# Kernel optimization log

Measured on AMD Instinct MI355X. Metric: run time of the kernel, lower is better.

## Reference

```python
import jax, jax.numpy as jnp
import numpy as np

B, L, D, H = 2, 2048, 1024, 16
DK = D // H
DFF = 4 * D
EPS = 1e-5  # torch LayerNorm default


def setup_inputs() -> dict:
    key = jax.random.key(0)
    ks = jax.random.split(key, 12)
    w = lambda k, shp: (jax.random.normal(k, shp, jnp.float32) * 0.02)
    return {
        "x": jax.random.normal(ks[0], (B, L, D), jnp.float32),
        "y": jax.random.normal(ks[1], (B, L, D), jnp.float32),
        "Wq": w(ks[2], (D, D)), "bq": jnp.zeros((D,), jnp.float32),
        "Wk": w(ks[3], (D, D)), "bk": jnp.zeros((D,), jnp.float32),
        "Wv": w(ks[4], (D, D)), "bv": jnp.zeros((D,), jnp.float32),
        "Wo": w(ks[5], (D, D)), "bo": jnp.zeros((D,), jnp.float32),
        "W1": w(ks[6], (D, DFF)), "b1": jnp.zeros((DFF,), jnp.float32),
        "W2": w(ks[7], (DFF, D)), "b2": jnp.zeros((D,), jnp.float32),
        "ln1_w": jnp.ones((L, D), jnp.float32), "ln1_b": jnp.zeros((L, D), jnp.float32),
        "ln2_w": jnp.ones((L, D), jnp.float32), "ln2_b": jnp.zeros((L, D), jnp.float32),
    }


def _layernorm2d(t, w, b):
    # nn.LayerNorm(normalized_shape=[L, D]): normalize jointly over last two dims
    mu = jnp.mean(t, axis=(-2, -1), keepdims=True)
    var = jnp.mean((t - mu) ** 2, axis=(-2, -1), keepdims=True)
    return (t - mu) * jax.lax.rsqrt(var + EPS) * w + b


def _attention(q_in, kv_in, Wq, bq, Wk, bk, Wv, bv, Wo, bo):
    split = lambda t: t.reshape(B, L, H, DK).transpose(0, 2, 1, 3)  # [B,H,L,DK]
    q = split(q_in @ Wq + bq)
    k = split(kv_in @ Wk + bk)
    v = split(kv_in @ Wv + bv)
    scores = jnp.einsum("bhqd,bhkd->bhqk", q, k) / (DK ** 0.5)
    # NOTE: original applies torch.tril to SCORES (zeroes upper triangle,
    # NOT -inf), so future positions still contribute exp(0)=1 in softmax.
    scores = jnp.tril(scores)
    p_attn = jax.nn.softmax(scores, axis=-1)
    out = jnp.einsum("bhqk,bhkd->bhqd", p_attn, v)
    out = out.transpose(0, 2, 1, 3).reshape(B, L, D)
    return out @ Wo + bo


def reference(x, y, Wq, bq, Wk, bk, Wv, bv, Wo, bo, W1, b1, W2, b2,
              ln1_w, ln1_b, ln2_w, ln2_b):
    # sublayer 0: pre-norm y, attention(query=x, key=value=norm(y)), residual
    y1 = y + _attention(x, _layernorm2d(y, ln1_w, ln1_b),
                        Wq, bq, Wk, bk, Wv, bv, Wo, bo)
    # sublayer 1: pre-norm, FFN (dropout inactive in eval), residual
    h = jax.nn.relu(_layernorm2d(y1, ln2_w, ln2_b) @ W1 + b1)
    return y1 + h @ W2 + b2
```

## Files before the change

### kernel.cpp

```cpp
#include <hip/hip_runtime.h>
#include <math.h>

#define B 2
#define L 2048
#define D 1024
#define H 16
#define DK 64
#define DFF 4096
#define EPS 1e-5f

typedef short short8 __attribute__((ext_vector_type(8)));
typedef short short4v __attribute__((ext_vector_type(4)));
typedef float float4v __attribute__((ext_vector_type(4)));
typedef unsigned int u32;

__device__ inline short f2bf(float f) {
    unsigned u = __builtin_bit_cast(unsigned, f);
    u += 0x7fffu + ((u >> 16) & 1u);
    return (short)(u >> 16);
}

__device__ inline float bf2f(short s) {
    unsigned u = ((unsigned)(unsigned short)s) << 16;
    return __builtin_bit_cast(float, u);
}

#define GLOAD_LDS16(gp, lp)                                                  \
    __builtin_amdgcn_global_load_lds(                                        \
        (const __attribute__((address_space(1))) u32*)(const void*)(gp),     \
        (__attribute__((address_space(3))) u32*)(void*)(lp), 16, 0, 0)

__device__ inline void xcd_remap(int& bx, int& by) {
    const int nbx = gridDim.x, nby = gridDim.y;
    const int orig = blockIdx.x + nbx * blockIdx.y;
    const int k = orig & 7, j = orig >> 3;
    const int nyc = nby >> 3;
    bx = j % nbx;
    by = k * nyc + j / nbx;
}


__global__ __launch_bounds__(256) void red_partial(const float* __restrict__ X,
                                                   float* __restrict__ part) {
    int b = blockIdx.y;
    const float4* p = (const float4*)(X + (size_t)b * L * D);
    float s = 0.f, ss = 0.f;
    for (int idx = blockIdx.x * 256 + threadIdx.x; idx < L * D / 4; idx += 256 * 256) {
        float4 v = p[idx];
        s += v.x + v.y + v.z + v.w;
        ss += v.x * v.x + v.y * v.y + v.z * v.z + v.w * v.w;
    }
    __shared__ float sh0[256], sh1[256];
    sh0[threadIdx.x] = s; sh1[threadIdx.x] = ss;
    __syncthreads();
    for (int o = 128; o; o >>= 1) {
        if (threadIdx.x < o) {
            sh0[threadIdx.x] += sh0[threadIdx.x + o];
            sh1[threadIdx.x] += sh1[threadIdx.x + o];
        }
        __syncthreads();
    }
    if (threadIdx.x == 0) {
        part[(b * 256 + blockIdx.x) * 2 + 0] = sh0[0];
        part[(b * 256 + blockIdx.x) * 2 + 1] = sh1[0];    }
}

__global__ __launch_bounds__(256) void red_final(const float* __restrict__ part,
                                                 float* __restrict__ stats) {
    int b = blockIdx.x;
    float s = part[(b * 256 + threadIdx.x) * 2 + 0];
    float ss = part[(b * 256 + threadIdx.x) * 2 + 1];
    __shared__ float sh0[256], sh1[256];
    sh0[threadIdx.x] = s; sh1[threadIdx.x] = ss;
    __syncthreads();
    for (int o = 128; o; o >>= 1) {
        if (threadIdx.x < o) {
            sh0[threadIdx.x] += sh0[threadIdx.x + o];
            sh1[threadIdx.x] += sh1[threadIdx.x + o];
        }
        __syncthreads();
    }
    if (threadIdx.x == 0) {
        const float invN = 1.f / (float)(L * D);
        float mu = sh0[0] * invN;
        float var = sh1[0] * invN - mu * mu;
        stats[b * 2 + 0] = mu;
        stats[b * 2 + 1] = rsqrtf(var + EPS);
    }
}

__global__ __launch_bounds__(256) void ln_apply_bf(const float* __restrict__ X,
                                                   const float* __restrict__ W,
                                                   const float* __restrict__ Bb,
                                                   const float* __restrict__ stats,
                                                   short* __restrict__ Yn) {
    int b = blockIdx.y;
    float mu = stats[b * 2 + 0];
    float rstd = stats[b * 2 + 1];
    size_t e = (size_t)(blockIdx.x * 256 + threadIdx.x) * 4;
    const float4 xv = *(const float4*)(X + (size_t)b * L * D + e);
    const float4 wv = *(const float4*)(W + e);
    const float4 bv = *(const float4*)(Bb + e);
    short4v o;
    o[0] = f2bf((xv.x - mu) * rstd * wv.x + bv.x);
    o[1] = f2bf((xv.y - mu) * rstd * wv.y + bv.y);
    o[2] = f2bf((xv.z - mu) * rstd * wv.z + bv.z);
    o[3] = f2bf((xv.w - mu) * rstd * wv.w + bv.w);
    *(short4v*)(Yn + (size_t)b * L * D + e) = o;
}

__global__ __launch_bounds__(256) void convert_bf(const float* __restrict__ X,
                                                  short* __restrict__ Y) {
    size_t e = (size_t)(blockIdx.x * 256 + threadIdx.x) * 4;
    const float4 v = *(const float4*)(X + e);
    short4v o = {f2bf(v.x), f2bf(v.y), f2bf(v.z), f2bf(v.w)};
    *(short4v*)(Y + e) = o;
}

__global__ __launch_bounds__(256) void wt_transpose(const float* __restrict__ W,
                                                    short* __restrict__ WT,
                                                    int K, int N) {
    __shared__ short tile[32][33];
    const int t = threadIdx.x;
    const int tx = t & 31, ty = t >> 5;
    const int k0 = blockIdx.y * 32, n0 = blockIdx.x * 32;
#pragma unroll
    for (int i = 0; i < 4; ++i) {
        const int k = ty + i * 8;
        tile[k][tx] = f2bf(W[(size_t)(k0 + k) * N + n0 + tx]);
    }
    __syncthreads();
#pragma unroll
    for (int i = 0; i < 4; ++i) {
        const int n = ty + i * 8;
        WT[(size_t)(n0 + n) * K + k0 + tx] = tile[tx][n];
    }
}


__global__ __launch_bounds__(256) void gemm_cv128(const short* __restrict__ A,
                                                  const short* __restrict__ BT,
                                                  const float* __restrict__ bias,
                                                  const float* __restrict__ Res,
                                                  void* __restrict__ Cout,
                                                  int M, int N, int K, int flags) {
    __shared__ short As[2][128 * 64];
    __shared__ short Bs[2][128 * 64];
    const int t = threadIdx.x;
    const int wave = t >> 6, lane = t & 63;
    const int m16 = lane & 15, q4 = lane >> 4;
    int bx, by;
    xcd_remap(bx, by);
    const int m0 = by * 128, n0 = bx * 128;
    const int wm = (wave >> 1) * 64, wn = (wave & 1) * 64;
    const int xorm = m16 & 7;

    float4v acc[4][4];
#pragma unroll
    for (int i = 0; i < 4; ++i)
#pragma unroll
        for (int j = 0; j < 4; ++j) acc[i][j] = (float4v){0.f, 0.f, 0.f, 0.f};

    auto stage = [&](int buf, int k0) {
#pragma unroll
        for (int p = 0; p < 4; ++p) {
            const int s = p * 256 + t;
            const int row = s >> 3;
            const int col = ((s & 7) ^ (row & 7)) * 8;
            short* lds = &As[buf][(p * 256 + wave * 64) * 8];
            GLOAD_LDS16(A + (size_t)(m0 + row) * K + k0 + col, lds);
        }
#pragma unroll
        for (int p = 0; p < 4; ++p) {
            const int s = p * 256 + t;
            const int row = s >> 3;
            const int col = ((s & 7) ^ (row & 7)) * 8;
            short* lds = &Bs[buf][(p * 256 + wave * 64) * 8];
            GLOAD_LDS16(BT + (size_t)(n0 + row) * K + k0 + col, lds);
        }
    };

    auto compute = [&](int buf) {
#pragma unroll
        for (int kk = 0; kk < 2; ++kk) {
            const int slot = ((kk * 4 + q4) ^ xorm) * 8;
            short8 af[4], bf[4];
#pragma unroll
            for (int mi = 0; mi < 4; ++mi)
                af[mi] = *(const short8*)&As[buf][(wm + mi * 16 + m16) * 64 + slot];
#pragma unroll
            for (int ni = 0; ni < 4; ++ni)
                bf[ni] = *(const short8*)&Bs[buf][(wn + ni * 16 + m16) * 64 + slot];
#pragma unroll
            for (int mi = 0; mi < 4; ++mi)
#pragma unroll
                for (int ni = 0; ni < 4; ++ni)
                    acc[mi][ni] = __builtin_amdgcn_mfma_f32_16x16x32_bf16(
                        af[mi], bf[ni], acc[mi][ni], 0, 0, 0);
        }
    };

    const int nt = K >> 6;
    stage(0, 0);
    for (int ti = 0; ti < nt; ++ti) {
        const int cur = ti & 1;
        if (ti + 1 < nt) {
            stage(cur ^ 1, (ti + 1) << 6);
            asm volatile("s_waitcnt vmcnt(8)" ::: "memory");
        } else {
            asm volatile("s_waitcnt vmcnt(0)" ::: "memory");
        }
        __builtin_amdgcn_s_barrier();
        __builtin_amdgcn_sched_barrier(0);
        compute(cur);
        __builtin_amdgcn_s_barrier();
    }

#pragma unroll
    for (int mi = 0; mi < 4; ++mi)
#pragma unroll
        for (int ni = 0; ni < 4; ++ni) {
            const int col = n0 + wn + ni * 16 + m16;
            const float bb = bias[col];
#pragma unroll
            for (int r = 0; r < 4; ++r) {
                const int row = m0 + wm + mi * 16 + q4 * 4 + r;
                float v = acc[mi][ni][r] + bb;
                if (Res) v += Res[(size_t)row * N + col];
                if (flags & 1) v = fmaxf(v, 0.f);
                if (flags & 2)
                    ((short*)Cout)[(size_t)row * N + col] = f2bf(v);
                else
                    ((float*)Cout)[(size_t)row * N + col] = v;
            }
        }
}

__global__ __launch_bounds__(512) void gemm_cv256(const short* __restrict__ A,
                                                  const short* __restrict__ BT,
                                                  const float* __restrict__ bias,
                                                  const float* __restrict__ Res,
                                                  void* __restrict__ Cout,
                                                  int M, int N, int K, int flags) {
    __shared__ short As[2][256 * 64];
    __shared__ short Bs[2][256 * 64];
    const int t = threadIdx.x;
    const int wave = t >> 6, lane = t & 63;
    const int m16 = lane & 15, q4 = lane >> 4;
    int bx, by;
    xcd_remap(bx, by);
    const int m0 = by * 256, n0 = bx * 256;
    const int wm = (wave >> 2) * 128, wn = (wave & 3) * 64;
    const int xorm = m16 & 7;

    float4v acc[8][4];
#pragma unroll
    for (int i = 0; i < 8; ++i)
#pragma unroll
        for (int j = 0; j < 4; ++j) acc[i][j] = (float4v){0.f, 0.f, 0.f, 0.f};

    auto stage = [&](int buf, int k0) {
#pragma unroll
        for (int p = 0; p < 4; ++p) {
            const int s = p * 512 + t;
            const int row = s >> 3;
            const int col = ((s & 7) ^ (row & 7)) * 8;
            short* lds = &As[buf][(p * 512 + wave * 64) * 8];
            GLOAD_LDS16(A + (size_t)(m0 + row) * K + k0 + col, lds);
        }
#pragma unroll
        for (int p = 0; p < 4; ++p) {
            const int s = p * 512 + t;
            const int row = s >> 3;
            const int col = ((s & 7) ^ (row & 7)) * 8;
            short* lds = &Bs[buf][(p * 512 + wave * 64) * 8];
            GLOAD_LDS16(BT + (size_t)(n0 + row) * K + k0 + col, lds);
        }
    };

    auto compute = [&](int buf) {
#pragma unroll
        for (int kk = 0; kk < 2; ++kk) {
            const int slot = ((kk * 4 + q4) ^ xorm) * 8;
            short8 af[8], bf[4];
#pragma unroll
            for (int mi = 0; mi < 8; ++mi)
                af[mi] = *(const short8*)&As[buf][(wm + mi * 16 + m16) * 64 + slot];
#pragma unroll
            for (int ni = 0; ni < 4; ++ni)
                bf[ni] = *(const short8*)&Bs[buf][(wn + ni * 16 + m16) * 64 + slot];
#pragma unroll
            for (int mi = 0; mi < 8; ++mi)
#pragma unroll
                for (int ni = 0; ni < 4; ++ni)
                    acc[mi][ni] = __builtin_amdgcn_mfma_f32_16x16x32_bf16(
                        af[mi], bf[ni], acc[mi][ni], 0, 0, 0);
        }
    };

    const int nt = K >> 6;
    stage(0, 0);
    for (int ti = 0; ti < nt; ++ti) {
        const int cur = ti & 1;
        if (ti + 1 < nt) {
            stage(cur ^ 1, (ti + 1) << 6);
            asm volatile("s_waitcnt vmcnt(8)" ::: "memory");
        } else {
            asm volatile("s_waitcnt vmcnt(0)" ::: "memory");
        }
        __builtin_amdgcn_s_barrier();
        __builtin_amdgcn_sched_barrier(0);
        compute(cur);
        __builtin_amdgcn_s_barrier();
    }

#pragma unroll
    for (int mi = 0; mi < 8; ++mi)
#pragma unroll
        for (int ni = 0; ni < 4; ++ni) {
            const int col = n0 + wn + ni * 16 + m16;
            const float bb = bias[col];
#pragma unroll
            for (int r = 0; r < 4; ++r) {
                const int row = m0 + wm + mi * 16 + q4 * 4 + r;
                float v = acc[mi][ni][r] + bb;
                if (Res) v += Res[(size_t)row * N + col];
                if (flags & 1) v = fmaxf(v, 0.f);
                if (flags & 2)
                    ((short*)Cout)[(size_t)row * N + col] = f2bf(v);
                else
                    ((float*)Cout)[(size_t)row * N + col] = v;
            }
        }
}


#define ASTR 72
#define SKV (2 * D)

__global__ __launch_bounds__(256) void v_tilesum(const short* __restrict__ KVg,
                                                 float* __restrict__ Vtile) {
    const int bh = blockIdx.x >> 5;
    const int kt = blockIdx.x & 31;
    const int b = bh >> 4, h = bh & (H - 1);
    const size_t baseV = (size_t)b * L * SKV + (size_t)h * DK + D;
    const int d = threadIdx.x & 63, g = threadIdx.x >> 6;
    float s = 0.f;
    for (int j = g * 16; j < g * 16 + 16; ++j)
        s += bf2f(KVg[baseV + (size_t)(kt * 64 + j) * SKV + d]);
    __shared__ float sh[4][64];
    sh[g][d] = s;
    __syncthreads();
    if (threadIdx.x < 64)
        Vtile[((size_t)bh * 32 + kt) * 64 + d] = sh[0][d] + sh[1][d] + sh[2][d] + sh[3][d];
}

__global__ __launch_bounds__(64) void v_suffix(const float* __restrict__ Vtile,
                                               float* __restrict__ Vsuf) {
    const int bh = blockIdx.x;
    const int d = threadIdx.x;
    float s = 0.f;
    Vsuf[((size_t)bh * 33 + 32) * 64 + d] = 0.f;
    for (int kt = 31; kt >= 0; --kt) {
        s += Vtile[((size_t)bh * 32 + kt) * 64 + d];
        Vsuf[((size_t)bh * 33 + kt) * 64 + d] = s;
    }
}


__device__ inline void attn_stage_load(const short* __restrict__ KVg,
                                       size_t baseK, int kt0, int sj, int sd8,
                                       short8* kr, short8* vr) {
#pragma unroll
    for (int rep = 0; rep < 2; ++rep) {
        const int j = rep * 32 + sj;
        const size_t g = baseK + (size_t)(kt0 + j) * SKV + sd8;
        kr[rep] = *(const short8*)(KVg + g);
        vr[rep] = *(const short8*)(KVg + g + D);
    }
}

__device__ inline void attn_stage_write(short* __restrict__ KbB,
                                        short* __restrict__ VtB,
                                        int sj, int sd8,
                                        const short8* kr, const short8* vr) {
    const int sm = sd8 >> 3;
#pragma unroll
    for (int rep = 0; rep < 2; ++rep) {
        const int j = rep * 32 + sj;
        *(short8*)&KbB[j * ASTR + sd8] = kr[rep];
        const int jsw = ((((j >> 3) ^ sm) << 3) | (j & 7));
#pragma unroll
        for (int i = 0; i < 8; ++i) VtB[(sd8 + i) * ASTR + jsw] = vr[rep][i];
    }
}

__global__ __launch_bounds__(256) void attn_mfma(const short* __restrict__ Qg,
                                                 const short* __restrict__ KVg,
                                                 const float* __restrict__ Vsuf,
                                                 short* __restrict__ O) {
    __shared__ alignas(16) short Kb[2][64 * ASTR];
    __shared__ alignas(16) short Vt[2][64 * ASTR];
    __shared__ alignas(16) short Pb[64 * ASTR];

    const int t = threadIdx.x;
    const int wave = t >> 6;
    const int lane = t & 63;
    const int m16 = lane & 15;
    const int q4 = lane >> 4;

    const int u = blockIdx.x & 15;
    const int bh = blockIdx.x >> 4;
    const int h = bh & (H - 1);
    const int b = bh >> 4;
    const size_t baseQ = (size_t)b * L * D + (size_t)h * DK;
    const size_t baseK = (size_t)b * L * SKV + (size_t)h * DK;

    const int sj = t >> 3;
    const int sd8 = (t & 7) * 8;

    const int irow = wave * 16 + m16;
    const int ig = irow >> 3;

#pragma unroll
    for (int pq = 0; pq < 2; ++pq) {
        const int qt = pq ? (31 - u) : u;
        const int q0 = qt * 64;
        const int rowA = q0 + wave * 16 + m16;

        short8 qf[2];
#pragma unroll
        for (int kc = 0; kc < 2; ++kc)
            qf[kc] = *(const short8*)(Qg + baseQ + (size_t)rowA * D + kc * 32 + q4 * 8);

        float lsum = 0.f;
        float4v acc[4];
#pragma unroll
        for (int f = 0; f < 4; ++f) acc[f] = (float4v){0.f, 0.f, 0.f, 0.f};

        {
            short8 kr[2], vr[2];
            attn_stage_load(KVg, baseK, 0, sj, sd8, kr, vr);
            attn_stage_write(&Kb[0][0], &Vt[0][0], sj, sd8, kr, vr);
        }
        __syncthreads();

        for (int kt = 0; kt <= qt; ++kt) {
            const int cur = kt & 1;
            const short* KbC = &Kb[cur][0];
            const short* VtC = &Vt[cur][0];

            short8 kr[2], vr[2];
            if (kt < qt)
                attn_stage_load(KVg, baseK, (kt + 1) * 64, sj, sd8, kr, vr);

            const bool diag = (kt == qt);

#pragma unroll
            for (int f = 0; f < 4; ++f) {
                const short8 kf0 = *(const short8*)&KbC[(f * 16 + m16) * ASTR + q4 * 8];
                const short8 kf1 = *(const short8*)&KbC[(f * 16 + m16) * ASTR + 32 + q4 * 8];
                float4v sv = {0.f, 0.f, 0.f, 0.f};
                sv = __builtin_amdgcn_mfma_f32_16x16x32_bf16(kf0, qf[0], sv, 0, 0, 0);
                sv = __builtin_amdgcn_mfma_f32_16x16x32_bf16(kf1, qf[1], sv, 0, 0, 0);

                float pv[4];
                if (diag) {
#pragma unroll
                    for (int r = 0; r < 4; ++r) {
                        const int jl = f * 16 + q4 * 4 + r;
                        pv[r] = (jl <= irow) ? __expf(sv[r] * 0.125f) : 1.0f;
                    }
                } else {
#pragma unroll
                    for (int r = 0; r < 4; ++r) pv[r] = __expf(sv[r] * 0.125f);
                }
                lsum += pv[0] + pv[1] + pv[2] + pv[3];

                short4v s4;
                s4[0] = f2bf(pv[0]); s4[1] = f2bf(pv[1]);
                s4[2] = f2bf(pv[2]); s4[3] = f2bf(pv[3]);
                const int jb = f * 2 + (q4 >> 1);
                *(short4v*)&Pb[irow * ASTR + (((jb ^ ig) << 3) | ((q4 & 1) << 2))] = s4;
            }

#pragma unroll
            for (int kc = 0; kc < 2; ++kc) {
                const short8 pf = *(const short8*)&Pb[irow * ASTR + (((kc * 4 + q4) ^ ig) << 3)];
#pragma unroll
                for (int f = 0; f < 4; ++f) {
                    const int d = f * 16 + m16;
                    const short8 vf = *(const short8*)&VtC[d * ASTR + (((kc * 4 + q4) ^ (d >> 3)) << 3)];
                    acc[f] = __builtin_amdgcn_mfma_f32_16x16x32_bf16(pf, vf, acc[f], 0, 0, 0);
                }
            }

            if (kt < qt)
                attn_stage_write(&Kb[cur ^ 1][0], &Vt[cur ^ 1][0], sj, sd8, kr, vr);
            __syncthreads();
        }

        float s = lsum;
        s += __shfl_xor(s, 16);
        s += __shfl_xor(s, 32);
        s += (float)(L - (qt + 1) * 64);
        const float inv = 1.0f / s;
        float invr[4];
#pragma unroll
        for (int r = 0; r < 4; ++r) invr[r] = __shfl(inv, q4 * 4 + r);

        const float* vs = Vsuf + ((size_t)bh * 33 + qt + 1) * 64;
#pragma unroll
        for (int f = 0; f < 4; ++f) {
            const float vadd = vs[f * 16 + m16];
#pragma unroll
            for (int r = 0; r < 4; ++r) {
                const int i = q0 + wave * 16 + q4 * 4 + r;
                O[baseQ + (size_t)i * D + f * 16 + m16] = f2bf((acc[f][r] + vadd) * invr[r]);
            }
        }
    }
}


extern "C" void kernel_launch(void* const* d_in, const int* in_sizes, int n_in,
                              void* d_out, int out_size, void* d_ws, size_t ws_size,
                              hipStream_t stream) {
    const float* x    = (const float*)d_in[0];
    const float* y    = (const float*)d_in[1];
    const float* Wq   = (const float*)d_in[2];
    const float* bq   = (const float*)d_in[3];
    const float* Wk   = (const float*)d_in[4];
    const float* bk   = (const float*)d_in[5];
    const float* Wv   = (const float*)d_in[6];
    const float* bv   = (const float*)d_in[7];
    const float* Wo   = (const float*)d_in[8];
    const float* bo   = (const float*)d_in[9];
    const float* W1   = (const float*)d_in[10];
    const float* b1   = (const float*)d_in[11];
    const float* W2   = (const float*)d_in[12];
    const float* b2   = (const float*)d_in[13];
    const float* ln1w = (const float*)d_in[14];
    const float* ln1b = (const float*)d_in[15];
    const float* ln2w = (const float*)d_in[16];
    const float* ln2b = (const float*)d_in[17];
    float* out = (float*)d_out;

    const size_t F = (size_t)B * L * D;
    char* p = (char*)d_ws;
    short* xb    = (short*)p; p += F * 2;
    short* ynb   = (short*)p; p += F * 2;
    short* qb    = (short*)p; p += F * 2;
    short* kvb   = (short*)p; p += 2 * F * 2;
    short* aob   = (short*)p; p += F * 2;
    short* y1nb  = (short*)p; p += F * 2;
    short* hb    = (short*)p; p += (size_t)B * L * DFF * 2;
    float* y1    = (float*)p; p += F * 4;
    short* WqT   = (short*)p; p += (size_t)D * D * 2;
    short* WkvT  = (short*)p; p += (size_t)D * 2 * D * 2;
    short* WoT   = (short*)p; p += (size_t)D * D * 2;
    short* W1T   = (short*)p; p += (size_t)D * DFF * 2;
    short* W2T   = (short*)p; p += (size_t)D * DFF * 2;
    float* biaskv= (float*)p; p += 2 * D * 4;
    float* vtile = (float*)p; p += (size_t)B * H * 32 * DK * 4;
    float* vsuf  = (float*)p; p += (size_t)B * H * 33 * DK * 4;
    float* part  = (float*)p; p += B * 256 * 2 * 4;
    float* stats = (float*)p;

    const int M = B * L;

    wt_transpose<<<dim3(D / 32, D / 32), 256, 0, stream>>>(Wq, WqT, D, D);
    wt_transpose<<<dim3(D / 32, D / 32), 256, 0, stream>>>(Wk, WkvT, D, D);
    wt_transpose<<<dim3(D / 32, D / 32), 256, 0, stream>>>(Wv, WkvT + (size_t)D * D, D, D);
    wt_transpose<<<dim3(D / 32, D / 32), 256, 0, stream>>>(Wo, WoT, D, D);
    wt_transpose<<<dim3(DFF / 32, D / 32), 256, 0, stream>>>(W1, W1T, D, DFF);
    wt_transpose<<<dim3(D / 32, DFF / 32), 256, 0, stream>>>(W2, W2T, DFF, D);
    hipMemcpyAsync(biaskv,     bk, D * sizeof(float), hipMemcpyDeviceToDevice, stream);
    hipMemcpyAsync(biaskv + D, bv, D * sizeof(float), hipMemcpyDeviceToDevice, stream);

    convert_bf<<<dim3(F / 1024), 256, 0, stream>>>(x, xb);

    red_partial<<<dim3(256, B), 256, 0, stream>>>(y, part);
    red_final<<<dim3(B), 256, 0, stream>>>(part, stats);
    ln_apply_bf<<<dim3(L * D / 1024, B), 256, 0, stream>>>(y, ln1w, ln1b, stats, ynb);

    gemm_cv128<<<dim3(D / 128, M / 128), 256, 0, stream>>>(xb, WqT, bq, nullptr, qb, M, D, D, 2);
    gemm_cv128<<<dim3(2 * D / 128, M / 128), 256, 0, stream>>>(ynb, WkvT, biaskv, nullptr, kvb, M, 2 * D, D, 2);

    v_tilesum<<<dim3(B * H * 32), 256, 0, stream>>>(kvb, vtile);
    v_suffix<<<dim3(B * H), 64, 0, stream>>>(vtile, vsuf);

    attn_mfma<<<dim3(B * H * 16), 256, 0, stream>>>(qb, kvb, vsuf, aob);

    gemm_cv128<<<dim3(D / 128, M / 128), 256, 0, stream>>>(aob, WoT, bo, y, y1, M, D, D, 0);

    red_partial<<<dim3(256, B), 256, 0, stream>>>(y1, part);
    red_final<<<dim3(B), 256, 0, stream>>>(part, stats);
    ln_apply_bf<<<dim3(L * D / 1024, B), 256, 0, stream>>>(y1, ln2w, ln2b, stats, y1nb);

    gemm_cv256<<<dim3(DFF / 256, M / 256), 512, 0, stream>>>(y1nb, W1T, b1, nullptr, hb, M, DFF, D, 3);

    gemm_cv128<<<dim3(D / 128, M / 128), 256, 0, stream>>>(hb, W2T, b2, y1, out, M, D, DFF, 0);
}
```

Before: 461.5 us.

## Merge Q and KV projections into one launch and split-K the W2 GEMM

Moves the GEMM tile body into a shared device function. The Q and KV projection GEMMs now run as a single 768-block launch with an XCD-aware block mapping, and the final FFN down-projection (K=4096) is split into two K halves across 512 blocks, followed by a small reduction kernel that adds the bias and residual. The aim is to fill the GPU better than the previous 256-block launches and to cut per-launch overhead. The cost is extra fp32 partial-sum traffic for the split-K, which reuses the qb/kvb scratch area, plus one more kernel launch.

Result: faster. 427.3 us (-7.4%).

```diff
diff --git a/kernel.cpp b/kernel.cpp
--- a/kernel.cpp
+++ b/kernel.cpp
@@ -62,7 +62,8 @@
     }
     if (threadIdx.x == 0) {
         part[(b * 256 + blockIdx.x) * 2 + 0] = sh0[0];
-        part[(b * 256 + blockIdx.x) * 2 + 1] = sh1[0];    }
+        part[(b * 256 + blockIdx.x) * 2 + 1] = sh1[0];
+    }
 }
 
 __global__ __launch_bounds__(256) void red_final(const float* __restrict__ part,
@@ -138,22 +139,21 @@
 }
 
 
-__global__ __launch_bounds__(256) void gemm_cv128(const short* __restrict__ A,
-                                                  const short* __restrict__ BT,
-                                                  const float* __restrict__ bias,
-                                                  const float* __restrict__ Res,
-                                                  void* __restrict__ Cout,
-                                                  int M, int N, int K, int flags) {
-    __shared__ short As[2][128 * 64];
-    __shared__ short Bs[2][128 * 64];
+__device__ __forceinline__ void cv128_body(const short* __restrict__ A,
+                                           const short* __restrict__ BT,
+                                           const float* __restrict__ bias,
+                                           const float* __restrict__ Res,
+                                           void* __restrict__ Cout,
+                                           int N, int Kloop, int lda, int flags,
+                                           int m0, int n0,
+                                           short* __restrict__ AsB,
+                                           short* __restrict__ BsB) {
     const int t = threadIdx.x;
     const int wave = t >> 6, lane = t & 63;
     const int m16 = lane & 15, q4 = lane >> 4;
-    int bx, by;
-    xcd_remap(bx, by);
-    const int m0 = by * 128, n0 = bx * 128;
     const int wm = (wave >> 1) * 64, wn = (wave & 1) * 64;
     const int xorm = m16 & 7;
+    const int BUFE = 128 * 64;
 
     float4v acc[4][4];
 #pragma unroll
@@ -162,35 +162,39 @@
         for (int j = 0; j < 4; ++j) acc[i][j] = (float4v){0.f, 0.f, 0.f, 0.f};
 
     auto stage = [&](int buf, int k0) {
+        short* AsBuf = AsB + buf * BUFE;
+        short* BsBuf = BsB + buf * BUFE;
 #pragma unroll
         for (int p = 0; p < 4; ++p) {
             const int s = p * 256 + t;
             const int row = s >> 3;
             const int col = ((s & 7) ^ (row & 7)) * 8;
-            short* lds = &As[buf][(p * 256 + wave * 64) * 8];
-            GLOAD_LDS16(A + (size_t)(m0 + row) * K + k0 + col, lds);
+            GLOAD_LDS16(A + (size_t)(m0 + row) * lda + k0 + col,
+                        AsBuf + (p * 256 + wave * 64) * 8);
         }
 #pragma unroll
         for (int p = 0; p < 4; ++p) {
             const int s = p * 256 + t;
             const int row = s >> 3;
             const int col = ((s & 7) ^ (row & 7)) * 8;
-            short* lds = &Bs[buf][(p * 256 + wave * 64) * 8];
-            GLOAD_LDS16(BT + (size_t)(n0 + row) * K + k0 + col, lds);
+            GLOAD_LDS16(BT + (size_t)(n0 + row) * lda + k0 + col,
+                        BsBuf + (p * 256 + wave * 64) * 8);
         }
     };
 
     auto compute = [&](int buf) {
+        const short* AsBuf = AsB + buf * BUFE;
+        const short* BsBuf = BsB + buf * BUFE;
 #pragma unroll
         for (int kk = 0; kk < 2; ++kk) {
             const int slot = ((kk * 4 + q4) ^ xorm) * 8;
             short8 af[4], bf[4];
 #pragma unroll
             for (int mi = 0; mi < 4; ++mi)
-                af[mi] = *(const short8*)&As[buf][(wm + mi * 16 + m16) * 64 + slot];
+                af[mi] = *(const short8*)&AsBuf[(wm + mi * 16 + m16) * 64 + slot];
 #pragma unroll
             for (int ni = 0; ni < 4; ++ni)
-                bf[ni] = *(const short8*)&Bs[buf][(wn + ni * 16 + m16) * 64 + slot];
+                bf[ni] = *(const short8*)&BsBuf[(wn + ni * 16 + m16) * 64 + slot];
 #pragma unroll
             for (int mi = 0; mi < 4; ++mi)
 #pragma unroll
@@ -200,7 +204,7 @@
         }
     };
 
-    const int nt = K >> 6;
+    const int nt = Kloop >> 6;
     stage(0, 0);
     for (int ti = 0; ti < nt; ++ti) {
         const int cur = ti & 1;
@@ -221,7 +225,7 @@
 #pragma unroll
         for (int ni = 0; ni < 4; ++ni) {
             const int col = n0 + wn + ni * 16 + m16;
-            const float bb = bias[col];
+            const float bb = bias ? bias[col] : 0.f;
 #pragma unroll
             for (int r = 0; r < 4; ++r) {
                 const int row = m0 + wm + mi * 16 + q4 * 4 + r;
@@ -234,6 +238,81 @@
                     ((float*)Cout)[(size_t)row * N + col] = v;
             }
         }
+}
+
+__global__ __launch_bounds__(256) void gemm_cv128(const short* __restrict__ A,
+                                                  const short* __restrict__ BT,
+                                                  const float* __restrict__ bias,
+                                                  const float* __restrict__ Res,
+                                                  void* __restrict__ Cout,
+                                                  int M, int N, int K, int flags) {
+    __shared__ short As[2][128 * 64];
+    __shared__ short Bs[2][128 * 64];
+    int bx, by;
+    xcd_remap(bx, by);
+    cv128_body(A, BT, bias, Res, Cout, N, K, K, flags, by * 128, bx * 128,
+               &As[0][0], &Bs[0][0]);
+}
+
+__global__ __launch_bounds__(256) void gemm_qkv(const short* __restrict__ xb,
+                                                const short* __restrict__ WqT,
+                                                const float* __restrict__ bq,
+                                                short* __restrict__ qb,
+                                                const short* __restrict__ ynb,
+                                                const short* __restrict__ WkvT,
+                                                const float* __restrict__ bkv,
+                                                short* __restrict__ kvb) {
+    __shared__ short As[2][128 * 64];
+    __shared__ short Bs[2][128 * 64];
+    const int id = blockIdx.x;
+    const int k = id & 7, j = id >> 3;
+    const int lin = k * 96 + j;
+    if (lin < 256) {
+        const int bx = lin & 7, by = lin >> 3;
+        cv128_body(xb, WqT, bq, nullptr, qb, 1024, 1024, 1024, 2,
+                   by * 128, bx * 128, &As[0][0], &Bs[0][0]);
+    } else {
+        const int l2 = lin - 256;
+        const int bx = l2 & 15, by = l2 >> 4;
+        cv128_body(ynb, WkvT, bkv, nullptr, kvb, 2048, 1024, 1024, 2,
+                   by * 128, bx * 128, &As[0][0], &Bs[0][0]);
+    }
+}
+
+__global__ __launch_bounds__(256) void gemm_cv128_sk(const short* __restrict__ A,
+                                                     const short* __restrict__ BT,
+                                                     float* __restrict__ part,
+                                                     int M, int N, int K) {
+    __shared__ short As[2][128 * 64];
+    __shared__ short Bs[2][128 * 64];
+    const int id = blockIdx.x;
+    const int k = id & 7, j = id >> 3;
+    const int lin = k * 64 + j;
+    const int ks = lin >> 8;
+    const int rem = lin & 255;
+    const int by = rem & 31, bx = (rem >> 5) & 7;
+    const int Kc = K >> 1;
+    cv128_body(A + ks * Kc, BT + ks * Kc, nullptr, nullptr,
+               part + (size_t)ks * M * N, N, Kc, K, 0,
+               by * 128, bx * 128, &As[0][0], &Bs[0][0]);
+}
+
+__global__ __launch_bounds__(256) void sk_reduce(const float* __restrict__ part,
+                                                 const float* __restrict__ bias,
+                                                 const float* __restrict__ Res,
+                                                 float* __restrict__ out,
+                                                 int MN, int N) {
+    const size_t e = (size_t)(blockIdx.x * 256 + threadIdx.x) * 4;
+    const float4 p0 = *(const float4*)(part + e);
+    const float4 p1 = *(const float4*)(part + (size_t)MN + e);
+    const float4 rv = *(const float4*)(Res + e);
+    const float4 bv = *(const float4*)(bias + (e & (size_t)(N - 1)));
+    float4 o;
+    o.x = p0.x + p1.x + rv.x + bv.x;
+    o.y = p0.y + p1.y + rv.y + bv.y;
+    o.z = p0.z + p1.z + rv.z + bv.z;
+    o.w = p0.w + p1.w + rv.w + bv.w;
+    *(float4*)(out + e) = o;
 }
 
 __global__ __launch_bounds__(512) void gemm_cv256(const short* __restrict__ A,
@@ -567,6 +646,8 @@
     float* part  = (float*)p; p += B * 256 * 2 * 4;
     float* stats = (float*)p;
 
+    float* skpart = (float*)qb;
+
     const int M = B * L;
 
     wt_transpose<<<dim3(D / 32, D / 32), 256, 0, stream>>>(Wq, WqT, D, D);
@@ -584,8 +665,7 @@
     red_final<<<dim3(B), 256, 0, stream>>>(part, stats);
     ln_apply_bf<<<dim3(L * D / 1024, B), 256, 0, stream>>>(y, ln1w, ln1b, stats, ynb);
 
-    gemm_cv128<<<dim3(D / 128, M / 128), 256, 0, stream>>>(xb, WqT, bq, nullptr, qb, M, D, D, 2);
-    gemm_cv128<<<dim3(2 * D / 128, M / 128), 256, 0, stream>>>(ynb, WkvT, biaskv, nullptr, kvb, M, 2 * D, D, 2);
+    gemm_qkv<<<dim3(768), 256, 0, stream>>>(xb, WqT, bq, qb, ynb, WkvT, biaskv, kvb);
 
     v_tilesum<<<dim3(B * H * 32), 256, 0, stream>>>(kvb, vtile);
     v_suffix<<<dim3(B * H), 64, 0, stream>>>(vtile, vsuf);
@@ -600,5 +680,6 @@
 
     gemm_cv256<<<dim3(DFF / 256, M / 256), 512, 0, stream>>>(y1nb, W1T, b1, nullptr, hb, M, DFF, D, 3);
 
-    gemm_cv128<<<dim3(D / 128, M / 128), 256, 0, stream>>>(hb, W2T, b2, y1, out, M, D, DFF, 0);
-}
+    gemm_cv128_sk<<<dim3(512), 256, 0, stream>>>(hb, W2T, skpart, M, D, DFF);
+    sk_reduce<<<dim3(M * D / 1024), 256, 0, stream>>>(skpart, b2, y1, out, M * D, D);
+}
```
